# Optimization experiments

Measured on AMD Instinct MI355X. Metric: run time of the kernel, lower is better.

The kernel has to match this reference:

```python
import jax, jax.numpy as jnp
import numpy as np
import math

N_NODES = 2000
LOOKBACK = 24
IN_DIM = 16
EMB_DIM = 64
BATCH = 32
LN_EPS = 1e-5


def _layernorm(v, g, b):
    mu = jnp.mean(v, axis=-1, keepdims=True)
    var = jnp.var(v, axis=-1, keepdims=True)
    return (v - mu) * jax.lax.rsqrt(var + LN_EPS) * g + b


def setup_inputs() -> dict:
    key = jax.random.key(0)
    ks = jax.random.split(key, 12)
    td = LOOKBACK * IN_DIM  # 384
    s_in = 1.0 / math.sqrt(td)
    s_d = 1.0 / math.sqrt(IN_DIM)
    return {
        "x": jax.random.normal(ks[0], (BATCH, N_NODES, LOOKBACK, IN_DIM), jnp.float32),
        "Wq": jax.random.normal(ks[1], (td, EMB_DIM), jnp.float32) * s_in,
        "bq": jax.random.normal(ks[2], (EMB_DIM,), jnp.float32) * 0.01,
        "Wk": jax.random.normal(ks[3], (td, EMB_DIM), jnp.float32) * s_in,
        "bk": jax.random.normal(ks[4], (EMB_DIM,), jnp.float32) * 0.01,
        "g0": jnp.ones((EMB_DIM,), jnp.float32),
        "beta0": jnp.zeros((EMB_DIM,), jnp.float32),
        "g1": jnp.ones((EMB_DIM,), jnp.float32),
        "beta1": jnp.zeros((EMB_DIM,), jnp.float32),
        "normal": jax.random.normal(ks[5], (N_NODES, LOOKBACK, IN_DIM), jnp.float32),
        "Win": jax.random.normal(ks[6], (IN_DIM, IN_DIM), jnp.float32) * s_d,
    }


def reference(x, Wq, bq, Wk, bk, g0, beta0, g1, beta1, normal, Win):
    b, n, t, d = x.shape
    xf = x.reshape(b, n, t * d)
    # per-sample q/k linear + layernorm (batched over b)
    q1 = _layernorm(xf @ Wq + bq, g0, beta0)  # (b, n, e)
    k1 = _layernorm(xf @ Wk + bk, g1, beta1)  # (b, n, e)
    # node-mixing attention: softmax(q k^T / sqrt(num_nodes)) @ normal
    scores = jnp.einsum('bne,bme->bnm', q1, k1) / math.sqrt(n)
    A = jax.nn.softmax(scores, axis=-1)  # (b, n, n)
    data = jnp.einsum('bnm,mf->bnf', A, normal.reshape(n, t * d)).reshape(b, n, t, d)
    # RPPsAtt attention weights over time (general attention, output_len = 1)
    query = x[:, :, -1, :] @ Win  # (b, n, d)
    att = jnp.einsum('bnd,bntd->bnt', query, data)  # scores vs context
    weight = jax.nn.softmax(att, axis=-1)  # (b, n, t)
    # res = stack(weights).permute(0,1,3,2) -> (b, n, t, 1), broadcast-add
    return data + weight[..., None]
```

## Files before the change

kernel.cpp:

```cpp
#include <hip/hip_runtime.h>
#include <math.h>

#define B_   32
#define NN   2000
#define NP   2048
#define TT   24
#define TD   384
#define EE   64
#define SCALE 0.022360679774997896f

typedef __bf16 bf16;
typedef __bf16 bf16x8 __attribute__((ext_vector_type(8)));
typedef float  f32x4  __attribute__((ext_vector_type(4)));

typedef __attribute__((address_space(3))) unsigned int       lds_u32;
typedef const __attribute__((address_space(1))) unsigned int g_u32;

__device__ __forceinline__ void dma16(const void* g, void* l) {
    __builtin_amdgcn_global_load_lds((g_u32*)g, (lds_u32*)l, 16, 0, 0);
}

__device__ __forceinline__ bool input_is_bf16(const void* g0) {
    return *reinterpret_cast<const unsigned short*>(g0) == 0x3F80;
}

__device__ __forceinline__ float safexp(float v) {
    return __expf(fminf(fmaxf(v, -30.f), 30.f));
}

__device__ __forceinline__ bf16x8 ld_frag(const bf16* p) {
    return *reinterpret_cast<const bf16x8*>(p);
}

__device__ __forceinline__ bf16x8 cvt8_f32(const float* p) {
    f32x4 a = *reinterpret_cast<const f32x4*>(p);
    f32x4 b = *reinterpret_cast<const f32x4*>(p + 4);
    bf16x8 r;
    r[0]=(bf16)a[0]; r[1]=(bf16)a[1]; r[2]=(bf16)a[2]; r[3]=(bf16)a[3];
    r[4]=(bf16)b[0]; r[5]=(bf16)b[1]; r[6]=(bf16)b[2]; r[7]=(bf16)b[3];
    return r;
}

__global__ void pack_w_k(const void* Wqv, const void* Wkv, bf16* __restrict__ Wp,
                         const void* gflag) {
    bool bf = input_is_bf16(gflag);
    int o = blockIdx.x * 256 + threadIdx.x;
    if (o >= 12*8*64*8) return;
    int j  = o & 7;
    int l  = (o >> 3) & 63;
    int nt = (o >> 9) & 7;
    int ks = o >> 12;
    int k   = ks*32 + ((l >> 4) * 8) + j;
    int col = nt*16 + (l & 15);
    float v;
    if (bf) v = (col < 64) ? (float)((const bf16*)Wqv)[k*64 + col]
                           : (float)((const bf16*)Wkv)[k*64 + col - 64];
    else    v = (col < 64) ? ((const float*)Wqv)[k*64 + col]
                           : ((const float*)Wkv)[k*64 + col - 64];
    Wp[o] = (bf16)v;
}

__global__ void pack_v_k(const void* normalv, bf16* __restrict__ Vp, const void* gflag) {
    bool bf = input_is_bf16(gflag);
    int o = blockIdx.x * 256 + threadIdx.x;
    if (o >= 64*24*512) return;
    int j  = o & 7;
    int l  = (o >> 3) & 63;
    int nt = (o >> 9) % 24;
    int kb = o / (24*512);
    int key = kb*32 + ((l >> 4) * 8) + j;
    int col = nt*16 + (l & 15);
    float v = 0.f;
    if (key < NN)
        v = bf ? (float)((const bf16*)normalv)[key*TD + col]
               : ((const float*)normalv)[key*TD + col];
    Vp[o] = (bf16)v;
}

__global__ void calc_query_k(const void* xv, const void* Winv, float* __restrict__ Qry,
                             const void* gflag) {
    bool bf = input_is_bf16(gflag);
    int o = blockIdx.x * 256 + threadIdx.x;
    if (o >= B_*NP*16) return;
    int d2 = o & 15;
    int n  = (o >> 4) & (NP - 1);
    int b  = o >> 15;
    float acc = 0.f;
    if (n < NN) {
        size_t xoff = ((size_t)(b*NN + n))*TD + (TT-1)*16;
        if (bf) {
            const bf16* xr = (const bf16*)xv + xoff;
            const bf16* Wn = (const bf16*)Winv;
            #pragma unroll
            for (int d = 0; d < 16; ++d) acc += (float)xr[d] * (float)Wn[d*16 + d2];
        } else {
            const float* xr = (const float*)xv + xoff;
            const float* Wn = (const float*)Winv;
            #pragma unroll
            for (int d = 0; d < 16; ++d) acc += xr[d] * Wn[d*16 + d2];
        }
    }
    Qry[o] = acc;
}

__global__ __launch_bounds__(256) void proj_ln_k(
        const void* xv, const bf16* __restrict__ Wp,
        const void* bqv, const void* bkv,
        const void* g0v, const void* be0v,
        const void* g1v, const void* be1v,
        bf16* __restrict__ Qb, bf16* __restrict__ Kp) {
    __shared__ __align__(16) bf16 Wbuf[2][4096];
    bool bf = input_is_bf16(g0v);
    int mb = blockIdx.x, b = blockIdx.y;
    int w    = threadIdx.x >> 6;
    int lane = threadIdx.x & 63;
    int quad = lane >> 4, lq = lane & 15;

    int rowA = mb*64 + w*16 + lq;
    int xrow = rowA < NN ? rowA : NN - 1;

    bf16x8 afr[12];
    if (bf) {
        const bf16* xp = (const bf16*)xv + ((size_t)(b*NN + xrow))*TD + quad*8;
        #pragma unroll
        for (int ks = 0; ks < 12; ++ks) afr[ks] = ld_frag(xp + ks*32);
    } else {
        const float* xp = (const float*)xv + ((size_t)(b*NN + xrow))*TD + quad*8;
        #pragma unroll
        for (int ks = 0; ks < 12; ++ks) afr[ks] = cvt8_f32(xp + ks*32);
    }

    auto stage = [&](int ks, int bufi) {
        const char* g = (const char*)Wp + (size_t)ks*8192;
        for (int c = w; c < 8; c += 4)
            dma16(g + c*1024 + (size_t)lane*16, &Wbuf[bufi][c*512]);
    };
    stage(0, 0);

    f32x4 acc[8];
    #pragma unroll
    for (int nt = 0; nt < 8; ++nt) acc[nt] = (f32x4){0.f, 0.f, 0.f, 0.f};
    __syncthreads();

    for (int ks = 0; ks < 12; ++ks) {
        int cur = ks & 1;
        if (ks + 1 < 12) stage(ks + 1, cur ^ 1);
        const bf16* wb = Wbuf[cur];
        #pragma unroll
        for (int nt = 0; nt < 8; ++nt) {
            bf16x8 bfr = ld_frag(wb + nt*512 + lane*8);
            acc[nt] = __builtin_amdgcn_mfma_f32_16x16x32_bf16(afr[ks], bfr, acc[nt], 0, 0, 0);
        }
        __syncthreads();
    }

    #pragma unroll
    for (int nt = 0; nt < 8; ++nt) {
        int c = nt*16 + lq;
        float bias;
        if (bf) bias = (c < 64) ? (float)((const bf16*)bqv)[c] : (float)((const bf16*)bkv)[c-64];
        else    bias = (c < 64) ? ((const float*)bqv)[c] : ((const float*)bkv)[c-64];
        #pragma unroll
        for (int r = 0; r < 4; ++r) acc[nt][r] += bias;
    }
    float outn[8][4];
    #pragma unroll
    for (int g = 0; g < 2; ++g) {
        float s[4], sq[4];
        #pragma unroll
        for (int r = 0; r < 4; ++r) {
            float p = 0.f, p2 = 0.f;
            #pragma unroll
            for (int nt = 0; nt < 4; ++nt) {
                float v = acc[g*4 + nt][r];
                p += v; p2 += v*v;
            }
            s[r] = p; sq[r] = p2;
        }
        #pragma unroll
        for (int m = 1; m < 16; m <<= 1) {
            #pragma unroll
            for (int r = 0; r < 4; ++r) {
                s[r]  += __shfl_xor(s[r],  m, 16);
                sq[r] += __shfl_xor(sq[r], m, 16);
            }
        }
        #pragma unroll
        for (int r = 0; r < 4; ++r) {
            float mean = s[r] * (1.f/64.f);
            float var  = fmaxf(sq[r] * (1.f/64.f) - mean*mean, 0.f);
            float rs   = rsqrtf(var + 1e-5f);
            #pragma unroll
            for (int nt = 0; nt < 4; ++nt) {
                int c = nt*16 + lq;
                float gv, bv;
                if (g == 0) { gv = bf ? (float)((const bf16*)g0v)[c] : ((const float*)g0v)[c];
                              bv = bf ? (float)((const bf16*)be0v)[c] : ((const float*)be0v)[c]; }
                else        { gv = bf ? (float)((const bf16*)g1v)[c] : ((const float*)g1v)[c];
                              bv = bf ? (float)((const bf16*)be1v)[c] : ((const float*)be1v)[c]; }
                outn[g*4 + nt][r] = (acc[g*4 + nt][r] - mean) * rs * gv + bv;
            }
        }
    }
    int rowq = mb*64 + w*16 + quad*4;
    #pragma unroll
    for (int r = 0; r < 4; ++r) {
        int row = rowq + r;
        bool real = row < NN;
        size_t qbase = ((size_t)(b*NP + row))*EE;
        int kb2  = row >> 5;
        int half = (row >> 4) & 1;
        int lqk  = row & 15;
        #pragma unroll
        for (int nt = 0; nt < 4; ++nt) {
            Qb[qbase + nt*16 + lq] = (bf16)(real ? outn[nt][r] : 0.f);
            int col   = nt*16 + lq;
            int f     = half*2 + (col >> 5);
            int quadk = (col >> 3) & 3;
            size_t idx = (((size_t)(b*64 + kb2)*4 + f)*64 + quadk*16 + lqk)*8 + (col & 7);
            Kp[idx] = (bf16)(real ? outn[4 + nt][r] : 0.f);
        }
    }
}

__global__ __launch_bounds__(512, 2) void attn_k(
        const bf16* __restrict__ Qb, const bf16* __restrict__ Kp,
        const bf16* __restrict__ Vp, const float* __restrict__ Qry,
        void* outv, const void* gflag) {
    __shared__ __align__(16) char SM[66560];
    bf16*  Kb    = (bf16*)(SM);
    bf16*  Vb    = (bf16*)(SM + 8192);
    bf16*  Pl    = (bf16*)(SM + 57344);
    bf16*  scr   = (bf16*)(SM);
    float* eBuf  = (float*)(SM + 52224);
    float* invD  = (float*)(SM + 65536);
    float* dnInv = (float*)(SM + 66048);

    bool bf = input_is_bf16(gflag);
    int mb = blockIdx.x, b = blockIdx.y;
    int w    = threadIdx.x >> 6;
    int lane = threadIdx.x & 63;
    int quad = lane >> 4, lq = lane & 15;
    int rowbase = mb*128;
    int myrow16 = rowbase + w*16;

    const bf16* qp = Qb + ((size_t)(b*NP + myrow16 + lq))*EE + quad*8;
    bf16x8 aq0 = ld_frag(qp);
    bf16x8 aq1 = ld_frag(qp + 32);

    f32x4 acc[8][3];
    #pragma unroll
    for (int rt = 0; rt < 8; ++rt)
        #pragma unroll
        for (int ct = 0; ct < 3; ++ct) acc[rt][ct] = (f32x4){0.f, 0.f, 0.f, 0.f};
    float den[4] = {0.f, 0.f, 0.f, 0.f};

    const bf16* kg = Kp + (size_t)(b*64)*2048;
    auto stage = [&](int kb, int bufi) {
        const char* kgb = (const char*)(kg + (size_t)kb*2048);
        const char* vgb = (const char*)(Vp + (size_t)kb*12288);
        for (int c = w; c < 28; c += 8) {
            if (c < 4) dma16(kgb + c*1024 + (size_t)lane*16, Kb + bufi*2048 + c*512);
            else       dma16(vgb + (size_t)(c-4)*1024 + (size_t)lane*16,
                             Vb + bufi*12288 + (c-4)*512);
        }
    };
    stage(0, 0);
    __syncthreads();

    for (int kb = 0; kb < 63; ++kb) {
        int cur = kb & 1;
        if (kb + 1 < 63) stage(kb + 1, cur ^ 1);

        const bf16* kc = Kb + cur*2048;
        bf16x8 bk0 = ld_frag(kc + lane*8);
        bf16x8 bk1 = ld_frag(kc +  512 + lane*8);
        bf16x8 bk2 = ld_frag(kc + 1024 + lane*8);
        bf16x8 bk3 = ld_frag(kc + 1536 + lane*8);
        f32x4 s0 = (f32x4){0.f,0.f,0.f,0.f}, s1 = (f32x4){0.f,0.f,0.f,0.f};
        s0 = __builtin_amdgcn_mfma_f32_16x16x32_bf16(aq0, bk0, s0, 0, 0, 0);
        s0 = __builtin_amdgcn_mfma_f32_16x16x32_bf16(aq1, bk1, s0, 0, 0, 0);
        s1 = __builtin_amdgcn_mfma_f32_16x16x32_bf16(aq0, bk2, s1, 0, 0, 0);
        s1 = __builtin_amdgcn_mfma_f32_16x16x32_bf16(aq1, bk3, s1, 0, 0, 0);

        int k0ok = (kb*32 + lq)      < NN;
        int k1ok = (kb*32 + 16 + lq) < NN;
        bf16* pw = Pl + w*512;
        int pb = (lq >> 3)*128 + quad*32 + (lq & 7);
        #pragma unroll
        for (int r = 0; r < 4; ++r) {
            float e0 = safexp(s0[r] * SCALE);
            float e1 = safexp(s1[r] * SCALE);
            den[r] += (k0ok ? e0 : 0.f) + (k1ok ? e1 : 0.f);
            pw[pb + r*8]       = (bf16)e0;
            pw[pb + 256 + r*8] = (bf16)e1;
        }

        const bf16* vc = Vb + cur*12288;
        bf16x8 bv0 = ld_frag(vc + (w*3 + 0)*512 + lane*8);
        bf16x8 bv1 = ld_frag(vc + (w*3 + 1)*512 + lane*8);
        bf16x8 bv2 = ld_frag(vc + (w*3 + 2)*512 + lane*8);

        asm volatile("s_waitcnt lgkmcnt(0)" ::: "memory");
        __builtin_amdgcn_s_barrier();
        asm volatile("" ::: "memory");
        __builtin_amdgcn_sched_barrier(0);

        #pragma unroll
        for (int rt = 0; rt < 8; ++rt) {
            bf16x8 ap = ld_frag(Pl + rt*512 + lane*8);
            acc[rt][0] = __builtin_amdgcn_mfma_f32_16x16x32_bf16(ap, bv0, acc[rt][0], 0, 0, 0);
            acc[rt][1] = __builtin_amdgcn_mfma_f32_16x16x32_bf16(ap, bv1, acc[rt][1], 0, 0, 0);
            acc[rt][2] = __builtin_amdgcn_mfma_f32_16x16x32_bf16(ap, bv2, acc[rt][2], 0, 0, 0);
        }
        __syncthreads();
    }

    #pragma unroll
    for (int r = 0; r < 4; ++r) {
        float s = den[r];
        s += __shfl_xor(s, 1, 16); s += __shfl_xor(s, 2, 16);
        s += __shfl_xor(s, 4, 16); s += __shfl_xor(s, 8, 16);
        den[r] = 1.f / fmaxf(s, 1e-30f);
    }
    if (lq == 0) {
        #pragma unroll
        for (int r = 0; r < 4; ++r) invD[w*16 + quad*4 + r] = den[r];
    }
    __syncthreads();

    const float* qryb = Qry + ((size_t)(b*NP + rowbase))*16 + lq;
    #pragma unroll
    for (int rt = 0; rt < 8; ++rt) {
        float inv[4], qd[4];
        #pragma unroll
        for (int r = 0; r < 4; ++r) {
            inv[r] = invD[rt*16 + quad*4 + r];
            qd[r]  = qryb[(size_t)(rt*16 + quad*4 + r)*16];
        }
        #pragma unroll
        for (int ct = 0; ct < 3; ++ct) {
            #pragma unroll
            for (int r = 0; r < 4; ++r) {
                float v = acc[rt][ct][r] * inv[r];
                acc[rt][ct][r] = v;
                float a = v * qd[r];
                a += __shfl_xor(a, 1, 16); a += __shfl_xor(a, 2, 16);
                a += __shfl_xor(a, 4, 16); a += __shfl_xor(a, 8, 16);
                float e = safexp(a);
                if (lq == 0) eBuf[(rt*16 + quad*4 + r)*26 + (w*3 + ct)] = e;
            }
        }
    }
    __syncthreads();

    if (lane < 16) {
        int row = w*16 + lane;
        float s = 0.f;
        #pragma unroll
        for (int t = 0; t < 24; ++t) s += eBuf[row*26 + t];
        dnInv[row] = 1.f / fmaxf(s, 1e-30f);
    }
    __syncthreads();

    if (bf) {
        #pragma unroll
        for (int half = 0; half < 2; ++half) {
            #pragma unroll
            for (int rti = 0; rti < 4; ++rti) {
                int rt = half*4 + rti;
                #pragma unroll
                for (int ct = 0; ct < 3; ++ct) {
                    int t = w*3 + ct;
                    #pragma unroll
                    for (int r = 0; r < 4; ++r) {
                        int row = rt*16 + quad*4 + r;
                        float wv = eBuf[row*26 + t] * dnInv[row];
                        float outv_ = (half ? acc[4 + rti][ct][r] : acc[rti][ct][r]) + wv;
                        scr[(size_t)(row - half*64)*408 + t*16 + lq] = (bf16)outv_;
                    }
                }
            }
            __syncthreads();
            bf16* og = (bf16*)outv + ((size_t)b*NN + rowbase + half*64)*TD;
            #pragma unroll
            for (int i = 0; i < 8; ++i) {
                int lrow = w*8 + i;
                int grow = rowbase + half*64 + lrow;
                if (grow < NN && lane < 48)
                    *reinterpret_cast<bf16x8*>(og + (size_t)lrow*TD + lane*8) =
                        *reinterpret_cast<const bf16x8*>(scr + (size_t)lrow*408 + lane*8);
            }
            __syncthreads();
        }
    } else {
        #pragma unroll
        for (int rt = 0; rt < 8; ++rt) {
            #pragma unroll
            for (int ct = 0; ct < 3; ++ct) {
                int t = w*3 + ct;
                #pragma unroll
                for (int r = 0; r < 4; ++r) {
                    int row  = rt*16 + quad*4 + r;
                    int grow = rowbase + row;
                    if (grow < NN) {
                        float wv = eBuf[row*26 + t] * dnInv[row];
                        ((float*)outv)[((size_t)(b*NN + grow))*TD + t*16 + lq] =
                            acc[rt][ct][r] + wv;
                    }
                }
            }
        }
    }
}

extern "C" void kernel_launch(void* const* d_in, const int* in_sizes, int n_in,
                              void* d_out, int out_size, void* d_ws, size_t ws_size,
                              hipStream_t stream) {
    const void* x      = d_in[0];
    const void* Wq     = d_in[1];
    const void* bq     = d_in[2];
    const void* Wk     = d_in[3];
    const void* bk     = d_in[4];
    const void* g0     = d_in[5];
    const void* be0    = d_in[6];
    const void* g1     = d_in[7];
    const void* be1    = d_in[8];
    const void* normal = d_in[9];
    const void* Win    = d_in[10];

    char* ws = (char*)d_ws;
    bf16*  Qb  = (bf16*)(ws);
    bf16*  Kp  = (bf16*)(ws + 8388608);
    bf16*  Vp  = (bf16*)(ws + 16777216);
    bf16*  Wp  = (bf16*)(ws + 16777216 + 1638400);
    float* Qry = (float*)(ws + 16777216 + 1638400 + 98304);

    pack_w_k<<<dim3(192), dim3(256), 0, stream>>>(Wq, Wk, Wp, g0);
    pack_v_k<<<dim3(3072), dim3(256), 0, stream>>>(normal, Vp, g0);
    calc_query_k<<<dim3(4096), dim3(256), 0, stream>>>(x, Win, Qry, g0);
    proj_ln_k<<<dim3(32, 32), dim3(256), 0, stream>>>(x, Wp, bq, bk, g0, be0, g1, be1, Qb, Kp);
    attn_k<<<dim3(16, 32), dim3(512), 0, stream>>>(Qb, Kp, Vp, Qry, d_out, g0);
}
```

Before: 412.1 us.

## Halve attention row tile and split key halves across warp pairs

Reduces the attention block tile from 128 to 64 query rows, doubling the grid, and has warp pairs compute the two 16-key halves of each score tile, merging softmax denominators through shared memory. Accumulator registers halve, allowing a higher occupancy hint and slightly less LDS. The aim is better CU fill and occupancy, at the cost of each K/V tile being streamed by twice as many blocks and less MFMA reuse per P fragment.

```diff
diff --git a/kernel.cpp b/kernel.cpp
--- a/kernel.cpp
+++ b/kernel.cpp
@@ -223,36 +223,37 @@
     }
 }
 
-__global__ __launch_bounds__(512, 2) void attn_k(
+__global__ __launch_bounds__(512, 4) void attn_k(
         const bf16* __restrict__ Qb, const bf16* __restrict__ Kp,
         const bf16* __restrict__ Vp, const float* __restrict__ Qry,
         void* outv, const void* gflag) {
-    __shared__ __align__(16) char SM[66560];
+    __shared__ __align__(16) char SM[61440];
     bf16*  Kb    = (bf16*)(SM);
     bf16*  Vb    = (bf16*)(SM + 8192);
     bf16*  Pl    = (bf16*)(SM + 57344);
     bf16*  scr   = (bf16*)(SM);
     float* eBuf  = (float*)(SM + 52224);
-    float* invD  = (float*)(SM + 65536);
-    float* dnInv = (float*)(SM + 66048);
+    float* denP  = (float*)(SM + 58880);
+    float* dnInv = (float*)(SM + 59392);
 
     bool bf = input_is_bf16(gflag);
     int mb = blockIdx.x, b = blockIdx.y;
     int w    = threadIdx.x >> 6;
     int lane = threadIdx.x & 63;
     int quad = lane >> 4, lq = lane & 15;
-    int rowbase = mb*128;
-    int myrow16 = rowbase + w*16;
-
-    const bf16* qp = Qb + ((size_t)(b*NP + myrow16 + lq))*EE + quad*8;
+    int rowbase = mb*64;
+    int rt = w >> 1;
+    int h  = w & 1;
+
+    const bf16* qp = Qb + ((size_t)(b*NP + rowbase + rt*16 + lq))*EE + quad*8;
     bf16x8 aq0 = ld_frag(qp);
     bf16x8 aq1 = ld_frag(qp + 32);
 
-    f32x4 acc[8][3];
-    #pragma unroll
-    for (int rt = 0; rt < 8; ++rt)
-        #pragma unroll
-        for (int ct = 0; ct < 3; ++ct) acc[rt][ct] = (f32x4){0.f, 0.f, 0.f, 0.f};
+    f32x4 acc[4][3];
+    #pragma unroll
+    for (int i = 0; i < 4; ++i)
+        #pragma unroll
+        for (int ct = 0; ct < 3; ++ct) acc[i][ct] = (f32x4){0.f, 0.f, 0.f, 0.f};
     float den[4] = {0.f, 0.f, 0.f, 0.f};
 
     const bf16* kg = Kp + (size_t)(b*64)*2048;
@@ -272,34 +273,27 @@
         int cur = kb & 1;
         if (kb + 1 < 63) stage(kb + 1, cur ^ 1);
 
-        const bf16* kc = Kb + cur*2048;
+        const bf16* kc = Kb + cur*2048 + h*1024;
         bf16x8 bk0 = ld_frag(kc + lane*8);
-        bf16x8 bk1 = ld_frag(kc +  512 + lane*8);
-        bf16x8 bk2 = ld_frag(kc + 1024 + lane*8);
-        bf16x8 bk3 = ld_frag(kc + 1536 + lane*8);
-        f32x4 s0 = (f32x4){0.f,0.f,0.f,0.f}, s1 = (f32x4){0.f,0.f,0.f,0.f};
-        s0 = __builtin_amdgcn_mfma_f32_16x16x32_bf16(aq0, bk0, s0, 0, 0, 0);
-        s0 = __builtin_amdgcn_mfma_f32_16x16x32_bf16(aq1, bk1, s0, 0, 0, 0);
-        s1 = __builtin_amdgcn_mfma_f32_16x16x32_bf16(aq0, bk2, s1, 0, 0, 0);
-        s1 = __builtin_amdgcn_mfma_f32_16x16x32_bf16(aq1, bk3, s1, 0, 0, 0);
-
-        int k0ok = (kb*32 + lq)      < NN;
-        int k1ok = (kb*32 + 16 + lq) < NN;
-        bf16* pw = Pl + w*512;
-        int pb = (lq >> 3)*128 + quad*32 + (lq & 7);
+        bf16x8 bk1 = ld_frag(kc + 512 + lane*8);
+        f32x4 s = (f32x4){0.f,0.f,0.f,0.f};
+        s = __builtin_amdgcn_mfma_f32_16x16x32_bf16(aq0, bk0, s, 0, 0, 0);
+        s = __builtin_amdgcn_mfma_f32_16x16x32_bf16(aq1, bk1, s, 0, 0, 0);
+
+        int kok = (kb*32 + h*16 + lq) < NN;
+        bf16* pw = Pl + rt*512;
+        int pb = (h*2 + (lq >> 3))*128 + quad*32 + (lq & 7);
         #pragma unroll
         for (int r = 0; r < 4; ++r) {
-            float e0 = safexp(s0[r] * SCALE);
-            float e1 = safexp(s1[r] * SCALE);
-            den[r] += (k0ok ? e0 : 0.f) + (k1ok ? e1 : 0.f);
-            pw[pb + r*8]       = (bf16)e0;
-            pw[pb + 256 + r*8] = (bf16)e1;
-        }
-
-        const bf16* vc = Vb + cur*12288;
-        bf16x8 bv0 = ld_frag(vc + (w*3 + 0)*512 + lane*8);
-        bf16x8 bv1 = ld_frag(vc + (w*3 + 1)*512 + lane*8);
-        bf16x8 bv2 = ld_frag(vc + (w*3 + 2)*512 + lane*8);
+            float e = safexp(s[r] * SCALE);
+            den[r] += kok ? e : 0.f;
+            pw[pb + r*8] = (bf16)e;
+        }
+
+        const bf16* vc = Vb + cur*12288 + (w*3)*512;
+        bf16x8 bv0 = ld_frag(vc + lane*8);
+        bf16x8 bv1 = ld_frag(vc +  512 + lane*8);
+        bf16x8 bv2 = ld_frag(vc + 1024 + lane*8);
 
         asm volatile("s_waitcnt lgkmcnt(0)" ::: "memory");
         __builtin_amdgcn_s_barrier();
@@ -307,11 +301,11 @@
         __builtin_amdgcn_sched_barrier(0);
 
         #pragma unroll
-        for (int rt = 0; rt < 8; ++rt) {
-            bf16x8 ap = ld_frag(Pl + rt*512 + lane*8);
-            acc[rt][0] = __builtin_amdgcn_mfma_f32_16x16x32_bf16(ap, bv0, acc[rt][0], 0, 0, 0);
-            acc[rt][1] = __builtin_amdgcn_mfma_f32_16x16x32_bf16(ap, bv1, acc[rt][1], 0, 0, 0);
-            acc[rt][2] = __builtin_amdgcn_mfma_f32_16x16x32_bf16(ap, bv2, acc[rt][2], 0, 0, 0);
+        for (int rt2 = 0; rt2 < 4; ++rt2) {
+            bf16x8 ap = ld_frag(Pl + rt2*512 + lane*8);
+            acc[rt2][0] = __builtin_amdgcn_mfma_f32_16x16x32_bf16(ap, bv0, acc[rt2][0], 0, 0, 0);
+            acc[rt2][1] = __builtin_amdgcn_mfma_f32_16x16x32_bf16(ap, bv1, acc[rt2][1], 0, 0, 0);
+            acc[rt2][2] = __builtin_amdgcn_mfma_f32_16x16x32_bf16(ap, bv2, acc[rt2][2], 0, 0, 0);
         }
         __syncthreads();
     }
@@ -321,41 +315,42 @@
         float s = den[r];
         s += __shfl_xor(s, 1, 16); s += __shfl_xor(s, 2, 16);
         s += __shfl_xor(s, 4, 16); s += __shfl_xor(s, 8, 16);
-        den[r] = 1.f / fmaxf(s, 1e-30f);
+        den[r] = s;
     }
     if (lq == 0) {
         #pragma unroll
-        for (int r = 0; r < 4; ++r) invD[w*16 + quad*4 + r] = den[r];
+        for (int r = 0; r < 4; ++r) denP[h*64 + rt*16 + quad*4 + r] = den[r];
     }
     __syncthreads();
 
     const float* qryb = Qry + ((size_t)(b*NP + rowbase))*16 + lq;
     #pragma unroll
-    for (int rt = 0; rt < 8; ++rt) {
+    for (int rt2 = 0; rt2 < 4; ++rt2) {
         float inv[4], qd[4];
         #pragma unroll
         for (int r = 0; r < 4; ++r) {
-            inv[r] = invD[rt*16 + quad*4 + r];
-            qd[r]  = qryb[(size_t)(rt*16 + quad*4 + r)*16];
+            int row = rt2*16 + quad*4 + r;
+            inv[r] = 1.f / fmaxf(denP[row] + denP[64 + row], 1e-30f);
+            qd[r]  = qryb[(size_t)row*16];
         }
         #pragma unroll
         for (int ct = 0; ct < 3; ++ct) {
             #pragma unroll
             for (int r = 0; r < 4; ++r) {
-                float v = acc[rt][ct][r] * inv[r];
-                acc[rt][ct][r] = v;
+                float v = acc[rt2][ct][r] * inv[r];
+                acc[rt2][ct][r] = v;
                 float a = v * qd[r];
                 a += __shfl_xor(a, 1, 16); a += __shfl_xor(a, 2, 16);
                 a += __shfl_xor(a, 4, 16); a += __shfl_xor(a, 8, 16);
                 float e = safexp(a);
-                if (lq == 0) eBuf[(rt*16 + quad*4 + r)*26 + (w*3 + ct)] = e;
+                if (lq == 0) eBuf[(rt2*16 + quad*4 + r)*26 + (w*3 + ct)] = e;
             }
         }
     }
     __syncthreads();
 
-    if (lane < 16) {
-        int row = w*16 + lane;
+    if (lane < 8) {
+        int row = w*8 + lane;
         float s = 0.f;
         #pragma unroll
         for (int t = 0; t < 24; ++t) s += eBuf[row*26 + t];
@@ -365,48 +360,42 @@
 
     if (bf) {
         #pragma unroll
-        for (int half = 0; half < 2; ++half) {
-            #pragma unroll
-            for (int rti = 0; rti < 4; ++rti) {
-                int rt = half*4 + rti;
-                #pragma unroll
-                for (int ct = 0; ct < 3; ++ct) {
-                    int t = w*3 + ct;
-                    #pragma unroll
-                    for (int r = 0; r < 4; ++r) {
-                        int row = rt*16 + quad*4 + r;
-                        float wv = eBuf[row*26 + t] * dnInv[row];
-                        float outv_ = (half ? acc[4 + rti][ct][r] : acc[rti][ct][r]) + wv;
-                        scr[(size_t)(row - half*64)*408 + t*16 + lq] = (bf16)outv_;
-                    }
-                }
-            }
-            __syncthreads();
-            bf16* og = (bf16*)outv + ((size_t)b*NN + rowbase + half*64)*TD;
-            #pragma unroll
-            for (int i = 0; i < 8; ++i) {
-                int lrow = w*8 + i;
-                int grow = rowbase + half*64 + lrow;
-                if (grow < NN && lane < 48)
-                    *reinterpret_cast<bf16x8*>(og + (size_t)lrow*TD + lane*8) =
-                        *reinterpret_cast<const bf16x8*>(scr + (size_t)lrow*408 + lane*8);
-            }
-            __syncthreads();
-        }
-    } else {
-        #pragma unroll
-        for (int rt = 0; rt < 8; ++rt) {
+        for (int rt2 = 0; rt2 < 4; ++rt2) {
             #pragma unroll
             for (int ct = 0; ct < 3; ++ct) {
                 int t = w*3 + ct;
                 #pragma unroll
                 for (int r = 0; r < 4; ++r) {
-                    int row  = rt*16 + quad*4 + r;
+                    int row = rt2*16 + quad*4 + r;
+                    float wv = eBuf[row*26 + t] * dnInv[row];
+                    scr[(size_t)row*408 + t*16 + lq] = (bf16)(acc[rt2][ct][r] + wv);
+                }
+            }
+        }
+        __syncthreads();
+        bf16* og = (bf16*)outv + ((size_t)b*NN + rowbase)*TD;
+        #pragma unroll
+        for (int i = 0; i < 8; ++i) {
+            int lrow = w*8 + i;
+            int grow = rowbase + lrow;
+            if (grow < NN && lane < 48)
+                *reinterpret_cast<bf16x8*>(og + (size_t)lrow*TD + lane*8) =
+                    *reinterpret_cast<const bf16x8*>(scr + (size_t)lrow*408 + lane*8);
+        }
+    } else {
+        #pragma unroll
+        for (int rt2 = 0; rt2 < 4; ++rt2) {
+            #pragma unroll
+            for (int ct = 0; ct < 3; ++ct) {
+                int t = w*3 + ct;
+                #pragma unroll
+                for (int r = 0; r < 4; ++r) {
+                    int row  = rt2*16 + quad*4 + r;
                     int grow = rowbase + row;
                     if (grow < NN) {
                         float wv = eBuf[row*26 + t] * dnInv[row];
                         ((float*)outv)[((size_t)(b*NN + grow))*TD + t*16 + lq] =
-                            acc[rt][ct][r] + wv;
+                            acc[rt2][ct][r] + wv;
                     }
                 }
             }
@@ -440,5 +429,5 @@
     pack_v_k<<<dim3(3072), dim3(256), 0, stream>>>(normal, Vp, g0);
     calc_query_k<<<dim3(4096), dim3(256), 0, stream>>>(x, Win, Qry, g0);
     proj_ln_k<<<dim3(32, 32), dim3(256), 0, stream>>>(x, Wp, bq, bk, g0, be0, g1, be1, Qb, Kp);
-    attn_k<<<dim3(16, 32), dim3(512), 0, stream>>>(Qb, Kp, Vp, Qry, d_out, g0);
-}
+    attn_k<<<dim3(32, 32), dim3(512), 0, stream>>>(Qb, Kp, Vp, Qry, d_out, g0);
+}
```

Result: faster. 387.1 us (-6.1%).
